# Optimization experiments

Hardware: AMD Instinct MI355X
Metric: run time of the kernel (lower is better)

Reference implementation:

```python
import jax, jax.numpy as jnp
import numpy as np
import math

B, C, H, W = 8, 64, 64, 64


def setup_inputs() -> dict:
    key = jax.random.key(0)
    k1, k2, k3, k4 = jax.random.split(key, 4)
    x = jax.random.normal(k1, (B, C, H, W), dtype=jnp.float32)
    fg_mask = jax.random.randint(k2, (B, 1, H, W), 0, 2, dtype=jnp.int32)
    w_qkv = jax.random.normal(k3, (3 * C, C), dtype=jnp.float32) * (1.0 / math.sqrt(C))
    w_proj = jax.random.normal(k4, (C, C), dtype=jnp.float32) * (1.0 / math.sqrt(C))
    b_proj = jnp.zeros((C,), dtype=jnp.float32)
    return {"x": x, "fg_mask": fg_mask, "w_qkv": w_qkv, "w_proj": w_proj, "b_proj": b_proj}


def reference(x, fg_mask, w_qkv, w_proj, b_proj):
    b, c, h, w = x.shape
    n = h * w
    # [B,C,H,W] -> [B,N,C]
    x_flat = x.reshape(b, c, n).transpose(0, 2, 1)
    qkv = x_flat @ w_qkv.T                      # [B,N,3C]
    q, k, v = jnp.split(qkv, 3, axis=-1)        # each [B,N,C]
    attn = jnp.einsum('bnc,bmc->bnm', q, k) / math.sqrt(c)  # [B,N,N]
    fg = fg_mask.reshape(b, n)                  # [B,N]
    attn = jnp.where(fg[:, None, :] == 0, -jnp.inf, attn)
    attn = jax.nn.softmax(attn, axis=-1)
    out = attn @ v                              # [B,N,C]
    out = out @ w_proj.T + b_proj               # [B,N,C]
    return out.transpose(0, 2, 1).reshape(b, c, h, w)
```

## Files before the change

kernel.cpp:

```cpp
#include <hip/hip_runtime.h>
#include <math.h>

#define Bdim 8
#define Cdim 64
#define Ndim 4096
#define TK   32
#define GNT  32

typedef __bf16 bf16x8 __attribute__((ext_vector_type(8)));
typedef __bf16 bf16x4 __attribute__((ext_vector_type(4)));
typedef float  f32x4  __attribute__((ext_vector_type(4)));

__device__ __forceinline__ void gload_lds16(const void* g, void* l) {
    __builtin_amdgcn_global_load_lds(
        (const __attribute__((address_space(1))) void*)g,
        (__attribute__((address_space(3))) void*)l, 16, 0, 0);
}

__device__ __forceinline__ float fexp2(float x) {
#if __has_builtin(__builtin_amdgcn_exp2f)
    return __builtin_amdgcn_exp2f(x);
#else
    return exp2f(x);
#endif
}

__global__ __launch_bounds__(256) void qkv_mfma_kernel(
    const float* __restrict__ x, const float* __restrict__ w_qkv,
    __bf16* __restrict__ Qb, __bf16* __restrict__ Kb, __bf16* __restrict__ Vb)
{
    __shared__ __align__(16) __bf16 whs[64 * 64];
    __shared__ __align__(16) __bf16 wls[64 * 64];
    __shared__ __align__(16) __bf16 tr[4][16 * 64];

    const int bx   = blockIdx.x;
    const int jc   = bx % 3;
    const int nblk = (bx / 3) & 63;
    const int b    = bx / 192;
    const int tid  = threadIdx.x;
    const int wv   = tid >> 6;
    const int l    = tid & 63;
    const int g    = l >> 4;
    const int li   = l & 15;
    const int nbase = nblk * 64 + wv * 16;

    const float KS = 0.125f * 1.44269504089f;

    {
        const float* wsrc = w_qkv + jc * 4096 + tid * 16;
        const float4 f0 = *(const float4*)(wsrc);
        const float4 f1 = *(const float4*)(wsrc + 4);
        const float4 f2 = *(const float4*)(wsrc + 8);
        const float4 f3 = *(const float4*)(wsrc + 12);
        const int row = tid >> 2;
        const int gb  = (tid & 3) * 2;
        bf16x8 h0, l0, h1, l1;
        const float* fp[4] = {(const float*)&f0, (const float*)&f1,
                              (const float*)&f2, (const float*)&f3};
#pragma unroll
        for (int q = 0; q < 2; ++q)
#pragma unroll
            for (int e = 0; e < 8; ++e) {
                const float v = fp[q * 2 + (e >> 2)][e & 3];
                const __bf16 h = (__bf16)v;
                if (q == 0) { h0[e] = h; l0[e] = (__bf16)(v - (float)h); }
                else        { h1[e] = h; l1[e] = (__bf16)(v - (float)h); }
            }
        *(bf16x8*)(whs + row * 64 + 8 * ((gb)     ^ (row & 7))) = h0;
        *(bf16x8*)(whs + row * 64 + 8 * ((gb + 1) ^ (row & 7))) = h1;
        *(bf16x8*)(wls + row * 64 + 8 * ((gb)     ^ (row & 7))) = l0;
        *(bf16x8*)(wls + row * 64 + 8 * ((gb + 1) ^ (row & 7))) = l1;
    }

    bf16x8 xhi[2], xlo[2];
#pragma unroll
    for (int kc = 0; kc < 2; ++kc)
#pragma unroll
        for (int jj = 0; jj < 8; ++jj) {
            const int c = kc * 32 + 8 * g + jj;
            const float v = x[((size_t)(b * 64 + c)) * Ndim + nbase + li];
            const __bf16 h = (__bf16)v;
            xhi[kc][jj] = h;
            xlo[kc][jj] = (__bf16)(v - (float)h);
        }
    __syncthreads();

    __bf16* trw = tr[wv];
    const float qs = (jc == 0) ? KS : 1.f;

#pragma unroll
    for (int jt = 0; jt < 4; ++jt) {
        const int rw = 16 * jt + li;
        const int rs = li & 7;
        const bf16x8 ah0 = *(const bf16x8*)(whs + rw * 64 + 8 * (g ^ rs));
        const bf16x8 ah1 = *(const bf16x8*)(whs + rw * 64 + 8 * ((4 + g) ^ rs));
        const bf16x8 al0 = *(const bf16x8*)(wls + rw * 64 + 8 * (g ^ rs));
        const bf16x8 al1 = *(const bf16x8*)(wls + rw * 64 + 8 * ((4 + g) ^ rs));
        f32x4 d = (f32x4){0.f, 0.f, 0.f, 0.f};
        d = __builtin_amdgcn_mfma_f32_16x16x32_bf16(ah0, xhi[0], d, 0, 0, 0);
        d = __builtin_amdgcn_mfma_f32_16x16x32_bf16(ah1, xhi[1], d, 0, 0, 0);
        d = __builtin_amdgcn_mfma_f32_16x16x32_bf16(ah0, xlo[0], d, 0, 0, 0);
        d = __builtin_amdgcn_mfma_f32_16x16x32_bf16(ah1, xlo[1], d, 0, 0, 0);
        d = __builtin_amdgcn_mfma_f32_16x16x32_bf16(al0, xhi[0], d, 0, 0, 0);
        d = __builtin_amdgcn_mfma_f32_16x16x32_bf16(al1, xhi[1], d, 0, 0, 0);

        if (jc == 2) {
#pragma unroll
            for (int r = 0; r < 4; ++r) {
                const int cv = jt * 16 + 4 * g + r;
                Vb[((size_t)(b * 64 + cv)) * Ndim + nbase + li] = (__bf16)d[r];
            }
        } else {
            bf16x4 pk;
#pragma unroll
            for (int r = 0; r < 4; ++r) pk[r] = (__bf16)(d[r] * qs);
            const int gran = (2 * jt + (g >> 1)) ^ (li & 7);
            *(bf16x4*)(trw + li * 64 + gran * 8 + 4 * (g & 1)) = pk;
        }
    }

    if (jc != 2) {
        __bf16* dstm = ((jc == 0) ? Qb : Kb) + ((size_t)b * Ndim + nbase) * 64;
#pragma unroll
        for (int p = 0; p < 2; ++p) {
            const int row = p * 8 + (l >> 3);
            const uint4 vr = *(const uint4*)(
                trw + row * 64 + ((l & 7) ^ (l >> 3)) * 8);
            *(uint4*)(dstm + row * 64 + 8 * (l & 7)) = vr;
        }
    }
}

__global__ __launch_bounds__(512, 4) void attn_kernel(
    const __bf16* __restrict__ Qb, const __bf16* __restrict__ Kb,
    const __bf16* __restrict__ Vb, const int* __restrict__ fg,
    const float* __restrict__ w_proj, const float* __restrict__ b_proj,
    float* __restrict__ out)
{
    __shared__ __align__(16) __bf16 kt[4][2][TK * 64];
    __shared__ __align__(16) __bf16 vt[4][2][64 * TK];
    __shared__ __align__(16) float  mtf[4][2][TK];

    const int bx   = blockIdx.x;
    const int b    = bx & 7;
    const int qblk = (bx >> 3) & 63;
    const int tid  = threadIdx.x;
    const int wv   = tid >> 6;
    const int grp  = wv >> 1;
    const int wsub = wv & 1;
    const int l    = tid & 63;
    const int g    = l >> 4;
    const int li   = l & 15;

    const int qlo = qblk * 64 + wsub * 32 + li;
    const __bf16* qb_lo = Qb + ((size_t)b * Ndim + qlo) * 64;
    const bf16x8 qa0 = *(const bf16x8*)(qb_lo + 8 * g);
    const bf16x8 qa1 = *(const bf16x8*)(qb_lo + 32 + 8 * g);
    const bf16x8 qa2 = *(const bf16x8*)(qb_lo + 16 * 64 + 8 * g);
    const bf16x8 qa3 = *(const bf16x8*)(qb_lo + 16 * 64 + 32 + 8 * g);

    const int kbase0 = grp * 1024;
    const __bf16* ksrcc[2];
    const __bf16* vsrcc[2];
    int kdst[2], vdst[2];
#pragma unroll
    for (int c = 0; c < 2; ++c) {
        const int R  = wsub * 16 + c * 8 + (l >> 3);
        const int kk = 8 * ((R >> 2) & 3) + 4 * (R >> 4) + (R & 3);
        ksrcc[c] = Kb + ((size_t)b * Ndim + kbase0 + kk) * 64 + 8 * ((l & 7) ^ (R & 7));
        kdst[c]  = (wsub * 16 + c * 8) * 64;
        const int row = wsub * 32 + c * 16 + (l >> 2);
        vsrcc[c] = Vb + ((size_t)(b * 64 + row)) * Ndim + kbase0
                 + 8 * ((l & 3) ^ ((row >> 1) & 3));
        vdst[c]  = (wsub * 32 + c * 16) * TK;
    }
    const int* fgp = fg + b * Ndim + kbase0;

    auto stage = [&](int t, int buf) {
#pragma unroll
        for (int c = 0; c < 2; ++c)
            gload_lds16(ksrcc[c] + (size_t)t * (TK * 64), &kt[grp][buf][kdst[c]]);
#pragma unroll
        for (int c = 0; c < 2; ++c)
            gload_lds16(vsrcc[c] + t * TK, &vt[grp][buf][vdst[c]]);
        if (wsub == 0 && l < TK)
            mtf[grp][buf][l] = fgp[t * TK + l] ? -12.f : -1e30f;
    };

    f32x4 accl[4], acch[4];
#pragma unroll
    for (int ct = 0; ct < 4; ++ct) {
        accl[ct] = (f32x4){0.f, 0.f, 0.f, 0.f};
        acch[ct] = (f32x4){0.f, 0.f, 0.f, 0.f};
    }
    f32x4 psv_l = (f32x4){0.f, 0.f, 0.f, 0.f};
    f32x4 psv_h = (f32x4){0.f, 0.f, 0.f, 0.f};

    stage(0, 0);

    for (int it = 0; it < GNT; ++it) {
        const int buf = it & 1;
        __syncthreads();
        if (it + 1 < GNT) stage(it + 1, buf ^ 1);

        const f32x4 mb0 = *(const f32x4*)(&mtf[grp][buf][8 * g]);
        const f32x4 mb1 = *(const f32x4*)(&mtf[grp][buf][8 * g + 4]);

        f32x4 s2l[2], s2h[2];
        __builtin_amdgcn_s_setprio(1);
#pragma unroll
        for (int st = 0; st < 2; ++st) {
            const int rb = (16 * st + li) * 64;
            const int sw = li & 7;
            const bf16x8 kb0 = *(const bf16x8*)(&kt[grp][buf][rb + 8 * (g ^ sw)]);
            const bf16x8 kb1 = *(const bf16x8*)(&kt[grp][buf][rb + 8 * ((4 + g) ^ sw)]);
            f32x4 zl = st ? mb1 : mb0;
            zl = __builtin_amdgcn_mfma_f32_16x16x32_bf16(kb0, qa0, zl, 0, 0, 0);
            zl = __builtin_amdgcn_mfma_f32_16x16x32_bf16(kb1, qa1, zl, 0, 0, 0);
            s2l[st] = zl;
            f32x4 zh = st ? mb1 : mb0;
            zh = __builtin_amdgcn_mfma_f32_16x16x32_bf16(kb0, qa2, zh, 0, 0, 0);
            zh = __builtin_amdgcn_mfma_f32_16x16x32_bf16(kb1, qa3, zh, 0, 0, 0);
            s2h[st] = zh;
        }
        __builtin_amdgcn_s_setprio(0);

#pragma unroll
        for (int st = 0; st < 2; ++st)
#pragma unroll
            for (int r = 0; r < 4; ++r) {
                const float el = fexp2(s2l[st][r]);
                const float eh = fexp2(s2h[st][r]);
                s2l[st][r] = el; psv_l[r] += el;
                s2h[st][r] = eh; psv_h[r] += eh;
            }

        bf16x8 pbl, pbh;
#pragma unroll
        for (int r = 0; r < 4; ++r) {
            pbl[r]     = (__bf16)s2l[0][r];
            pbl[4 + r] = (__bf16)s2l[1][r];
            pbh[r]     = (__bf16)s2h[0][r];
            pbh[4 + r] = (__bf16)s2h[1][r];
        }

        __builtin_amdgcn_s_setprio(1);
#pragma unroll
        for (int ct = 0; ct < 4; ++ct) {
            const int c = 16 * ct + li;
            const bf16x8 vf = *(const bf16x8*)(
                &vt[grp][buf][c * TK + 8 * (g ^ ((li >> 1) & 3))]);
            accl[ct] = __builtin_amdgcn_mfma_f32_16x16x32_bf16(vf, pbl, accl[ct], 0, 0, 0);
            acch[ct] = __builtin_amdgcn_mfma_f32_16x16x32_bf16(vf, pbh, acch[ct], 0, 0, 0);
        }
        __builtin_amdgcn_s_setprio(0);
    }

    float lsum_l = (psv_l[0] + psv_l[1]) + (psv_l[2] + psv_l[3]);
    float lsum_h = (psv_h[0] + psv_h[1]) + (psv_h[2] + psv_h[3]);
    lsum_l += __shfl_xor(lsum_l, 16);
    lsum_l += __shfl_xor(lsum_l, 32);
    lsum_h += __shfl_xor(lsum_h, 16);
    lsum_h += __shfl_xor(lsum_h, 32);

    float* mlb = (float*)&kt[0][0][0];
    __syncthreads();

    auto chunk = [&](int cidx) -> float* {
        return (cidx < 4) ? (float*)&vt[0][0][0] + cidx * 2048
                          : mlb + 256 + (cidx - 4) * 2048;
    };

    if (grp > 0) {
        const int p = grp - 1;
        if (g == 0) {
            mlb[((p * 2 + wsub) * 2 + 0) * 16 + li] = lsum_l;
            mlb[((p * 2 + wsub) * 2 + 1) * 16 + li] = lsum_h;
        }
        float* o = chunk(p * 2 + wsub);
#pragma unroll
        for (int fi = 0; fi < 8; ++fi)
            *(f32x4*)(o + (fi * 64 + l) * 4) = (fi < 4) ? accl[fi] : acch[fi - 4];
    }
    __syncthreads();
    if (grp > 0) return;

    float Ltl = lsum_l, Lth = lsum_h;
#pragma unroll
    for (int p = 0; p < 3; ++p) {
        Ltl += mlb[((p * 2 + wsub) * 2 + 0) * 16 + li];
        Lth += mlb[((p * 2 + wsub) * 2 + 1) * 16 + li];
    }
    const float invl = 1.f / Ltl, invh = 1.f / Lth;

    bf16x8 ob01l, ob23l, ob01h, ob23h;
#pragma unroll
    for (int fi = 0; fi < 8; ++fi) {
        const int  ct = fi & 3;
        const bool hi = fi >= 4;
        f32x4 s = hi ? acch[ct] : accl[ct];
#pragma unroll
        for (int p = 0; p < 3; ++p) {
            const f32x4 v = *(const f32x4*)(chunk(p * 2 + wsub) + (fi * 64 + l) * 4);
#pragma unroll
            for (int r = 0; r < 4; ++r) s[r] += v[r];
        }
        const float inv = hi ? invh : invl;
#pragma unroll
        for (int r = 0; r < 4; ++r) {
            const __bf16 o = (__bf16)(s[r] * inv);
            if (fi == 0) ob01l[r] = o;
            else if (fi == 1) ob01l[4 + r] = o;
            else if (fi == 2) ob23l[r] = o;
            else if (fi == 3) ob23l[4 + r] = o;
            else if (fi == 4) ob01h[r] = o;
            else if (fi == 5) ob01h[4 + r] = o;
            else if (fi == 6) ob23h[r] = o;
            else              ob23h[4 + r] = o;
        }
    }

    const int nbase = qblk * 64 + wsub * 32;
#pragma unroll
    for (int cot = 0; cot < 4; ++cot) {
        const int co = 16 * cot + li;
        const float* wr = w_proj + co * 64;
        const float4 f0 = *(const float4*)(wr + 4 * g);
        const float4 f1 = *(const float4*)(wr + 16 + 4 * g);
        const float4 f2 = *(const float4*)(wr + 32 + 4 * g);
        const float4 f3 = *(const float4*)(wr + 48 + 4 * g);
        bf16x8 wf0, wf1;
        wf0[0] = (__bf16)f0.x; wf0[1] = (__bf16)f0.y; wf0[2] = (__bf16)f0.z; wf0[3] = (__bf16)f0.w;
        wf0[4] = (__bf16)f1.x; wf0[5] = (__bf16)f1.y; wf0[6] = (__bf16)f1.z; wf0[7] = (__bf16)f1.w;
        wf1[0] = (__bf16)f2.x; wf1[1] = (__bf16)f2.y; wf1[2] = (__bf16)f2.z; wf1[3] = (__bf16)f2.w;
        wf1[4] = (__bf16)f3.x; wf1[5] = (__bf16)f3.y; wf1[6] = (__bf16)f3.z; wf1[7] = (__bf16)f3.w;

        f32x4 yl = (f32x4){0.f, 0.f, 0.f, 0.f};
        yl = __builtin_amdgcn_mfma_f32_16x16x32_bf16(wf0, ob01l, yl, 0, 0, 0);
        yl = __builtin_amdgcn_mfma_f32_16x16x32_bf16(wf1, ob23l, yl, 0, 0, 0);
        f32x4 yh = (f32x4){0.f, 0.f, 0.f, 0.f};
        yh = __builtin_amdgcn_mfma_f32_16x16x32_bf16(wf0, ob01h, yh, 0, 0, 0);
        yh = __builtin_amdgcn_mfma_f32_16x16x32_bf16(wf1, ob23h, yh, 0, 0, 0);

        const f32x4 bp = *(const f32x4*)(b_proj + 16 * cot + 4 * g);
#pragma unroll
        for (int r = 0; r < 4; ++r) {
            const int co_s = 16 * cot + 4 * g + r;
            float* orow = out + ((size_t)(b * 64 + co_s)) * Ndim + nbase;
            orow[li]      = yl[r] + bp[r];
            orow[16 + li] = yh[r] + bp[r];
        }
    }
}

extern "C" void kernel_launch(void* const* d_in, const int* in_sizes, int n_in,
                              void* d_out, int out_size, void* d_ws, size_t ws_size,
                              hipStream_t stream) {
    const float* x      = (const float*)d_in[0];
    const int*   fg     = (const int*)d_in[1];
    const float* w_qkv  = (const float*)d_in[2];
    const float* w_proj = (const float*)d_in[3];
    const float* b_proj = (const float*)d_in[4];
    float* out = (float*)d_out;

    const size_t per = (size_t)Bdim * Cdim * Ndim;
    __bf16* Qb = (__bf16*)d_ws;
    __bf16* Kb = Qb + per;
    __bf16* Vb = Kb + per;

    qkv_mfma_kernel<<<dim3(Bdim * (Ndim / 64) * 3), dim3(256), 0, stream>>>(
        x, w_qkv, Qb, Kb, Vb);
    attn_kernel<<<dim3(Bdim * (Ndim / 64)), dim3(512), 0, stream>>>(
        Qb, Kb, Vb, fg, w_proj, b_proj, out);
}
```

Before: 61.25 us.

## Switch attention MFMAs to 32x32x16 tiles and precompute mask bias in QKV kernel

Rewrites the attention inner loop to use 32x32x16 bf16 MFMA instructions instead of pairs of 16x16x32 ones, reorganizing Q/K/V fragment loads, the K row permutation, the accumulators and the projection epilogue to match. The foreground mask is converted once to a float bias in the QKV kernel and streamed into LDS by async global-to-LDS loads, replacing per-tile int loads and selects. The aim is fewer MFMA issues and less VGPR shuffling per tile; the cost is a different register layout and an extra workspace buffer.

```diff
diff --git a/kernel.cpp b/kernel.cpp
--- a/kernel.cpp
+++ b/kernel.cpp
@@ -10,6 +10,7 @@
 typedef __bf16 bf16x8 __attribute__((ext_vector_type(8)));
 typedef __bf16 bf16x4 __attribute__((ext_vector_type(4)));
 typedef float  f32x4  __attribute__((ext_vector_type(4)));
+typedef float  f32x16 __attribute__((ext_vector_type(16)));
 
 __device__ __forceinline__ void gload_lds16(const void* g, void* l) {
     __builtin_amdgcn_global_load_lds(
@@ -27,7 +28,9 @@
 
 __global__ __launch_bounds__(256) void qkv_mfma_kernel(
     const float* __restrict__ x, const float* __restrict__ w_qkv,
-    __bf16* __restrict__ Qb, __bf16* __restrict__ Kb, __bf16* __restrict__ Vb)
+    const int* __restrict__ fg,
+    __bf16* __restrict__ Qb, __bf16* __restrict__ Kb, __bf16* __restrict__ Vb,
+    float* __restrict__ fgb)
 {
     __shared__ __align__(16) __bf16 whs[64 * 64];
     __shared__ __align__(16) __bf16 wls[64 * 64];
@@ -45,6 +48,11 @@
     const int nbase = nblk * 64 + wv * 16;
 
     const float KS = 0.125f * 1.44269504089f;
+
+    if (jc == 1 && tid < 64) {
+        const int n = nblk * 64 + tid;
+        fgb[b * Ndim + n] = fg[b * Ndim + n] ? -12.f : -1e30f;
+    }
 
     {
         const float* wsrc = w_qkv + jc * 4096 + tid * 16;
@@ -58,13 +66,13 @@
         const float* fp[4] = {(const float*)&f0, (const float*)&f1,
                               (const float*)&f2, (const float*)&f3};
 #pragma unroll
-        for (int q = 0; q < 2; ++q)
+        for (int qq = 0; qq < 2; ++qq)
 #pragma unroll
             for (int e = 0; e < 8; ++e) {
-                const float v = fp[q * 2 + (e >> 2)][e & 3];
+                const float v = fp[qq * 2 + (e >> 2)][e & 3];
                 const __bf16 h = (__bf16)v;
-                if (q == 0) { h0[e] = h; l0[e] = (__bf16)(v - (float)h); }
-                else        { h1[e] = h; l1[e] = (__bf16)(v - (float)h); }
+                if (qq == 0) { h0[e] = h; l0[e] = (__bf16)(v - (float)h); }
+                else         { h1[e] = h; l1[e] = (__bf16)(v - (float)h); }
             }
         *(bf16x8*)(whs + row * 64 + 8 * ((gb)     ^ (row & 7))) = h0;
         *(bf16x8*)(whs + row * 64 + 8 * ((gb + 1) ^ (row & 7))) = h1;
@@ -133,7 +141,7 @@
 
 __global__ __launch_bounds__(512, 4) void attn_kernel(
     const __bf16* __restrict__ Qb, const __bf16* __restrict__ Kb,
-    const __bf16* __restrict__ Vb, const int* __restrict__ fg,
+    const __bf16* __restrict__ Vb, const float* __restrict__ fgb,
     const float* __restrict__ w_proj, const float* __restrict__ b_proj,
     float* __restrict__ out)
 {
@@ -149,52 +157,46 @@
     const int grp  = wv >> 1;
     const int wsub = wv & 1;
     const int l    = tid & 63;
-    const int g    = l >> 4;
-    const int li   = l & 15;
-
-    const int qlo = qblk * 64 + wsub * 32 + li;
-    const __bf16* qb_lo = Qb + ((size_t)b * Ndim + qlo) * 64;
-    const bf16x8 qa0 = *(const bf16x8*)(qb_lo + 8 * g);
-    const bf16x8 qa1 = *(const bf16x8*)(qb_lo + 32 + 8 * g);
-    const bf16x8 qa2 = *(const bf16x8*)(qb_lo + 16 * 64 + 8 * g);
-    const bf16x8 qa3 = *(const bf16x8*)(qb_lo + 16 * 64 + 32 + 8 * g);
+    const int q    = l & 31;
+    const int hi   = l >> 5;
+
+    const int qrow = qblk * 64 + wsub * 32 + q;
+    const __bf16* qbp = Qb + ((size_t)b * Ndim + qrow) * 64;
+    bf16x8 qf[4];
+#pragma unroll
+    for (int s = 0; s < 4; ++s)
+        qf[s] = *(const bf16x8*)(qbp + 16 * s + 8 * hi);
 
     const int kbase0 = grp * 1024;
     const __bf16* ksrcc[2];
     const __bf16* vsrcc[2];
     int kdst[2], vdst[2];
 #pragma unroll
-    for (int c = 0; c < 2; ++c) {
-        const int R  = wsub * 16 + c * 8 + (l >> 3);
-        const int kk = 8 * ((R >> 2) & 3) + 4 * (R >> 4) + (R & 3);
-        ksrcc[c] = Kb + ((size_t)b * Ndim + kbase0 + kk) * 64 + 8 * ((l & 7) ^ (R & 7));
-        kdst[c]  = (wsub * 16 + c * 8) * 64;
-        const int row = wsub * 32 + c * 16 + (l >> 2);
-        vsrcc[c] = Vb + ((size_t)(b * 64 + row)) * Ndim + kbase0
-                 + 8 * ((l & 3) ^ ((row >> 1) & 3));
-        vdst[c]  = (wsub * 32 + c * 16) * TK;
-    }
-    const int* fgp = fg + b * Ndim + kbase0;
+    for (int cc = 0; cc < 2; ++cc) {
+        const int R  = wsub * 16 + cc * 8 + (l >> 3);
+        const int pi = (R & 19) | ((R & 4) << 1) | ((R & 8) >> 1);
+        ksrcc[cc] = Kb + ((size_t)b * Ndim + kbase0 + pi) * 64 + 8 * ((l & 7) ^ (R & 7));
+        kdst[cc]  = (wsub * 16 + cc * 8) * 64;
+        const int row = wsub * 32 + cc * 16 + (l >> 2);
+        vsrcc[cc] = Vb + ((size_t)(b * 64 + row)) * Ndim + kbase0
+                  + 8 * ((l & 3) ^ ((row >> 1) & 3));
+        vdst[cc]  = (wsub * 32 + cc * 16) * TK;
+    }
+    const float* fgbp = fgb + b * Ndim + kbase0;
 
     auto stage = [&](int t, int buf) {
 #pragma unroll
-        for (int c = 0; c < 2; ++c)
-            gload_lds16(ksrcc[c] + (size_t)t * (TK * 64), &kt[grp][buf][kdst[c]]);
-#pragma unroll
-        for (int c = 0; c < 2; ++c)
-            gload_lds16(vsrcc[c] + t * TK, &vt[grp][buf][vdst[c]]);
-        if (wsub == 0 && l < TK)
-            mtf[grp][buf][l] = fgp[t * TK + l] ? -12.f : -1e30f;
+        for (int cc = 0; cc < 2; ++cc)
+            gload_lds16(ksrcc[cc] + (size_t)t * (TK * 64), &kt[grp][buf][kdst[cc]]);
+#pragma unroll
+        for (int cc = 0; cc < 2; ++cc)
+            gload_lds16(vsrcc[cc] + t * TK, &vt[grp][buf][vdst[cc]]);
+        if (wsub == 0 && l < 8)
+            gload_lds16(fgbp + t * 32 + l * 4, &mtf[grp][buf][0]);
     };
 
-    f32x4 accl[4], acch[4];
-#pragma unroll
-    for (int ct = 0; ct < 4; ++ct) {
-        accl[ct] = (f32x4){0.f, 0.f, 0.f, 0.f};
-        acch[ct] = (f32x4){0.f, 0.f, 0.f, 0.f};
-    }
-    f32x4 psv_l = (f32x4){0.f, 0.f, 0.f, 0.f};
-    f32x4 psv_h = (f32x4){0.f, 0.f, 0.f, 0.f};
+    f32x16 acc0 = {}, acc1 = {};
+    f32x4  psv  = {};
 
     stage(0, 0);
 
@@ -203,65 +205,59 @@
         __syncthreads();
         if (it + 1 < GNT) stage(it + 1, buf ^ 1);
 
-        const f32x4 mb0 = *(const f32x4*)(&mtf[grp][buf][8 * g]);
-        const f32x4 mb1 = *(const f32x4*)(&mtf[grp][buf][8 * g + 4]);
-
-        f32x4 s2l[2], s2h[2];
+        const float* mrow = &mtf[grp][buf][0];
+        const f32x4 ma = *(const f32x4*)(mrow + 8 * hi);
+        const f32x4 mb = *(const f32x4*)(mrow + 8 * hi + 4);
+        const f32x4 mc = *(const f32x4*)(mrow + 16 + 8 * hi);
+        const f32x4 md = *(const f32x4*)(mrow + 20 + 8 * hi);
+        f32x16 z;
+#pragma unroll
+        for (int r = 0; r < 4; ++r) {
+            z[r] = ma[r]; z[4 + r] = mb[r]; z[8 + r] = mc[r]; z[12 + r] = md[r];
+        }
+
         __builtin_amdgcn_s_setprio(1);
 #pragma unroll
-        for (int st = 0; st < 2; ++st) {
-            const int rb = (16 * st + li) * 64;
-            const int sw = li & 7;
-            const bf16x8 kb0 = *(const bf16x8*)(&kt[grp][buf][rb + 8 * (g ^ sw)]);
-            const bf16x8 kb1 = *(const bf16x8*)(&kt[grp][buf][rb + 8 * ((4 + g) ^ sw)]);
-            f32x4 zl = st ? mb1 : mb0;
-            zl = __builtin_amdgcn_mfma_f32_16x16x32_bf16(kb0, qa0, zl, 0, 0, 0);
-            zl = __builtin_amdgcn_mfma_f32_16x16x32_bf16(kb1, qa1, zl, 0, 0, 0);
-            s2l[st] = zl;
-            f32x4 zh = st ? mb1 : mb0;
-            zh = __builtin_amdgcn_mfma_f32_16x16x32_bf16(kb0, qa2, zh, 0, 0, 0);
-            zh = __builtin_amdgcn_mfma_f32_16x16x32_bf16(kb1, qa3, zh, 0, 0, 0);
-            s2h[st] = zh;
+        for (int s = 0; s < 4; ++s) {
+            const bf16x8 kf = *(const bf16x8*)(
+                &kt[grp][buf][q * 64 + 8 * ((hi + 2 * s) ^ (q & 7))]);
+            z = __builtin_amdgcn_mfma_f32_32x32x16_bf16(kf, qf[s], z, 0, 0, 0);
         }
         __builtin_amdgcn_s_setprio(0);
 
-#pragma unroll
-        for (int st = 0; st < 2; ++st)
-#pragma unroll
-            for (int r = 0; r < 4; ++r) {
-                const float el = fexp2(s2l[st][r]);
-                const float eh = fexp2(s2h[st][r]);
-                s2l[st][r] = el; psv_l[r] += el;
-                s2h[st][r] = eh; psv_h[r] += eh;
-            }
-
-        bf16x8 pbl, pbh;
-#pragma unroll
-        for (int r = 0; r < 4; ++r) {
-            pbl[r]     = (__bf16)s2l[0][r];
-            pbl[4 + r] = (__bf16)s2l[1][r];
-            pbh[r]     = (__bf16)s2h[0][r];
-            pbh[4 + r] = (__bf16)s2h[1][r];
+        f32x16 p;
+#pragma unroll
+        for (int r = 0; r < 16; ++r) {
+            p[r] = fexp2(z[r]);
+            psv[r & 3] += p[r];
+        }
+        bf16x8 pb0, pb1;
+#pragma unroll
+        for (int j = 0; j < 8; ++j) {
+            pb0[j] = (__bf16)p[j];
+            pb1[j] = (__bf16)p[8 + j];
         }
 
         __builtin_amdgcn_s_setprio(1);
 #pragma unroll
-        for (int ct = 0; ct < 4; ++ct) {
-            const int c = 16 * ct + li;
-            const bf16x8 vf = *(const bf16x8*)(
-                &vt[grp][buf][c * TK + 8 * (g ^ ((li >> 1) & 3))]);
-            accl[ct] = __builtin_amdgcn_mfma_f32_16x16x32_bf16(vf, pbl, accl[ct], 0, 0, 0);
-            acch[ct] = __builtin_amdgcn_mfma_f32_16x16x32_bf16(vf, pbh, acch[ct], 0, 0, 0);
+        for (int h = 0; h < 2; ++h) {
+            const int c   = 32 * h + q;
+            const int csw = (c >> 1) & 3;
+            const bf16x8 vf0 = *(const bf16x8*)(&vt[grp][buf][c * 32 + 8 * ((hi)     ^ csw)]);
+            const bf16x8 vf1 = *(const bf16x8*)(&vt[grp][buf][c * 32 + 8 * ((hi + 2) ^ csw)]);
+            if (h == 0) {
+                acc0 = __builtin_amdgcn_mfma_f32_32x32x16_bf16(vf0, pb0, acc0, 0, 0, 0);
+                acc0 = __builtin_amdgcn_mfma_f32_32x32x16_bf16(vf1, pb1, acc0, 0, 0, 0);
+            } else {
+                acc1 = __builtin_amdgcn_mfma_f32_32x32x16_bf16(vf0, pb0, acc1, 0, 0, 0);
+                acc1 = __builtin_amdgcn_mfma_f32_32x32x16_bf16(vf1, pb1, acc1, 0, 0, 0);
+            }
         }
         __builtin_amdgcn_s_setprio(0);
     }
 
-    float lsum_l = (psv_l[0] + psv_l[1]) + (psv_l[2] + psv_l[3]);
-    float lsum_h = (psv_h[0] + psv_h[1]) + (psv_h[2] + psv_h[3]);
-    lsum_l += __shfl_xor(lsum_l, 16);
-    lsum_l += __shfl_xor(lsum_l, 32);
-    lsum_h += __shfl_xor(lsum_h, 16);
-    lsum_h += __shfl_xor(lsum_h, 32);
+    float lsum = (psv[0] + psv[1]) + (psv[2] + psv[3]);
+    lsum += __shfl_xor(lsum, 32);
 
     float* mlb = (float*)&kt[0][0][0];
     __syncthreads();
@@ -272,83 +268,76 @@
     };
 
     if (grp > 0) {
-        const int p = grp - 1;
-        if (g == 0) {
-            mlb[((p * 2 + wsub) * 2 + 0) * 16 + li] = lsum_l;
-            mlb[((p * 2 + wsub) * 2 + 1) * 16 + li] = lsum_h;
-        }
-        float* o = chunk(p * 2 + wsub);
-#pragma unroll
-        for (int fi = 0; fi < 8; ++fi)
-            *(f32x4*)(o + (fi * 64 + l) * 4) = (fi < 4) ? accl[fi] : acch[fi - 4];
+        const int pp = grp - 1;
+        if (l < 32) mlb[(pp * 2 + wsub) * 32 + l] = lsum;
+        float* o = chunk(pp * 2 + wsub);
+#pragma unroll
+        for (int fi = 0; fi < 8; ++fi) {
+            f32x4 v;
+#pragma unroll
+            for (int e = 0; e < 4; ++e)
+                v[e] = (fi < 4) ? acc0[(fi & 3) * 4 + e] : acc1[(fi & 3) * 4 + e];
+            *(f32x4*)(o + (fi * 64 + l) * 4) = v;
+        }
     }
     __syncthreads();
     if (grp > 0) return;
 
-    float Ltl = lsum_l, Lth = lsum_h;
-#pragma unroll
-    for (int p = 0; p < 3; ++p) {
-        Ltl += mlb[((p * 2 + wsub) * 2 + 0) * 16 + li];
-        Lth += mlb[((p * 2 + wsub) * 2 + 1) * 16 + li];
-    }
-    const float invl = 1.f / Ltl, invh = 1.f / Lth;
-
-    bf16x8 ob01l, ob23l, ob01h, ob23h;
-#pragma unroll
-    for (int fi = 0; fi < 8; ++fi) {
-        const int  ct = fi & 3;
-        const bool hi = fi >= 4;
-        f32x4 s = hi ? acch[ct] : accl[ct];
-#pragma unroll
-        for (int p = 0; p < 3; ++p) {
-            const f32x4 v = *(const f32x4*)(chunk(p * 2 + wsub) + (fi * 64 + l) * 4);
-#pragma unroll
-            for (int r = 0; r < 4; ++r) s[r] += v[r];
-        }
-        const float inv = hi ? invh : invl;
-#pragma unroll
-        for (int r = 0; r < 4; ++r) {
-            const __bf16 o = (__bf16)(s[r] * inv);
-            if (fi == 0) ob01l[r] = o;
-            else if (fi == 1) ob01l[4 + r] = o;
-            else if (fi == 2) ob23l[r] = o;
-            else if (fi == 3) ob23l[4 + r] = o;
-            else if (fi == 4) ob01h[r] = o;
-            else if (fi == 5) ob01h[4 + r] = o;
-            else if (fi == 6) ob23h[r] = o;
-            else              ob23h[4 + r] = o;
-        }
-    }
-
-    const int nbase = qblk * 64 + wsub * 32;
-#pragma unroll
-    for (int cot = 0; cot < 4; ++cot) {
-        const int co = 16 * cot + li;
-        const float* wr = w_proj + co * 64;
-        const float4 f0 = *(const float4*)(wr + 4 * g);
-        const float4 f1 = *(const float4*)(wr + 16 + 4 * g);
-        const float4 f2 = *(const float4*)(wr + 32 + 4 * g);
-        const float4 f3 = *(const float4*)(wr + 48 + 4 * g);
-        bf16x8 wf0, wf1;
-        wf0[0] = (__bf16)f0.x; wf0[1] = (__bf16)f0.y; wf0[2] = (__bf16)f0.z; wf0[3] = (__bf16)f0.w;
-        wf0[4] = (__bf16)f1.x; wf0[5] = (__bf16)f1.y; wf0[6] = (__bf16)f1.z; wf0[7] = (__bf16)f1.w;
-        wf1[0] = (__bf16)f2.x; wf1[1] = (__bf16)f2.y; wf1[2] = (__bf16)f2.z; wf1[3] = (__bf16)f2.w;
-        wf1[4] = (__bf16)f3.x; wf1[5] = (__bf16)f3.y; wf1[6] = (__bf16)f3.z; wf1[7] = (__bf16)f3.w;
-
-        f32x4 yl = (f32x4){0.f, 0.f, 0.f, 0.f};
-        yl = __builtin_amdgcn_mfma_f32_16x16x32_bf16(wf0, ob01l, yl, 0, 0, 0);
-        yl = __builtin_amdgcn_mfma_f32_16x16x32_bf16(wf1, ob23l, yl, 0, 0, 0);
-        f32x4 yh = (f32x4){0.f, 0.f, 0.f, 0.f};
-        yh = __builtin_amdgcn_mfma_f32_16x16x32_bf16(wf0, ob01h, yh, 0, 0, 0);
-        yh = __builtin_amdgcn_mfma_f32_16x16x32_bf16(wf1, ob23h, yh, 0, 0, 0);
-
-        const f32x4 bp = *(const f32x4*)(b_proj + 16 * cot + 4 * g);
-#pragma unroll
-        for (int r = 0; r < 4; ++r) {
-            const int co_s = 16 * cot + 4 * g + r;
-            float* orow = out + ((size_t)(b * 64 + co_s)) * Ndim + nbase;
-            orow[li]      = yl[r] + bp[r];
-            orow[16 + li] = yh[r] + bp[r];
+    float Lt = lsum;
+#pragma unroll
+    for (int pp = 0; pp < 3; ++pp)
+        Lt += mlb[(pp * 2 + wsub) * 32 + q];
+    const float inv = 1.f / Lt;
+
+    f32x16 m0 = acc0, m1 = acc1;
+#pragma unroll
+    for (int pp = 0; pp < 3; ++pp) {
+        const float* o = chunk(pp * 2 + wsub);
+#pragma unroll
+        for (int fi = 0; fi < 8; ++fi) {
+            const f32x4 v = *(const f32x4*)(o + (fi * 64 + l) * 4);
+#pragma unroll
+            for (int e = 0; e < 4; ++e) {
+                if (fi < 4) m0[(fi & 3) * 4 + e] += v[e];
+                else        m1[(fi & 3) * 4 + e] += v[e];
+            }
+        }
+    }
+
+    bf16x8 ob[4];
+#pragma unroll
+    for (int s = 0; s < 4; ++s)
+#pragma unroll
+        for (int j = 0; j < 8; ++j) {
+            const float vv = (s < 2) ? m0[j + 8 * (s & 1)] : m1[j + 8 * (s & 1)];
+            ob[s][j] = (__bf16)(vv * inv);
+        }
+
+    const int nb = qblk * 64 + wsub * 32;
+#pragma unroll
+    for (int H = 0; H < 2; ++H) {
+        const int co = 32 * H + q;
+        f32x16 y = {};
+#pragma unroll
+        for (int s = 0; s < 4; ++s) {
+            const float* wr = w_proj + co * 64 + 4 * hi + 16 * s;
+            const float4 fA = *(const float4*)(wr);
+            const float4 fB = *(const float4*)(wr + 8);
+            bf16x8 wf;
+            wf[0] = (__bf16)fA.x; wf[1] = (__bf16)fA.y;
+            wf[2] = (__bf16)fA.z; wf[3] = (__bf16)fA.w;
+            wf[4] = (__bf16)fB.x; wf[5] = (__bf16)fB.y;
+            wf[6] = (__bf16)fB.z; wf[7] = (__bf16)fB.w;
+            y = __builtin_amdgcn_mfma_f32_32x32x16_bf16(wf, ob[s], y, 0, 0, 0);
+        }
+#pragma unroll
+        for (int rq = 0; rq < 4; ++rq) {
+            const f32x4 bp = *(const f32x4*)(b_proj + 32 * H + 4 * hi + 8 * rq);
+#pragma unroll
+            for (int e = 0; e < 4; ++e) {
+                const int co2 = 32 * H + e + 8 * rq + 4 * hi;
+                out[((size_t)(b * 64 + co2)) * Ndim + nb + q] = y[rq * 4 + e] + bp[e];
+            }
         }
     }
 }
@@ -364,12 +353,13 @@
     float* out = (float*)d_out;
 
     const size_t per = (size_t)Bdim * Cdim * Ndim;
-    __bf16* Qb = (__bf16*)d_ws;
-    __bf16* Kb = Qb + per;
-    __bf16* Vb = Kb + per;
+    __bf16* Qb  = (__bf16*)d_ws;
+    __bf16* Kb  = Qb + per;
+    __bf16* Vb  = Kb + per;
+    float*  fgb = (float*)(Vb + per);
 
     qkv_mfma_kernel<<<dim3(Bdim * (Ndim / 64) * 3), dim3(256), 0, stream>>>(
-        x, w_qkv, Qb, Kb, Vb);
+        x, w_qkv, fg, Qb, Kb, Vb, fgb);
     attn_kernel<<<dim3(Bdim * (Ndim / 64)), dim3(512), 0, stream>>>(
-        Qb, Kb, Vb, fg, w_proj, b_proj, out);
-}
+        Qb, Kb, Vb, fgb, w_proj, b_proj, out);
+}
```

After: 62.39 us. No clear change (+1.9%).
